# Kernel tuning notes

Hardware: AMD Instinct MI355X
Metric: run time of the kernel (lower is better)

## Reference

```python
import jax, jax.numpy as jnp
import numpy as np

MASK_GROUP = 8
RATIO = 0.125
K = max(1, min(MASK_GROUP, round(RATIO * MASK_GROUP)))  # = 1


def sparify_mask(outM):
    # top-k over the mask_group axis, scatter 1.0 at top-k positions
    _, idx = jax.lax.top_k(outM, K)              # [..., K]
    oh = jax.nn.one_hot(idx, outM.shape[-1], dtype=outM.dtype)  # [..., K, G]
    return jnp.sum(oh, axis=-2)                   # [..., G] 0/1 mask


def setup_inputs() -> dict:
    key = jax.random.key(0)
    ks = jax.random.split(key, 7)
    B, S, D, F = 4, 2048, 2048, 8192
    stdv = 1.0 / np.sqrt(F)
    u = lambda k, shape: jax.random.uniform(k, shape, jnp.float32, -stdv, stdv)
    return {
        "x": jax.random.normal(ks[0], (B, S, D), jnp.float32),
        "W1": u(ks[1], (F, D)),
        "b1": u(ks[2], (F,)),
        "Wm": u(ks[3], (MASK_GROUP, D)),
        "bm": u(ks[4], (MASK_GROUP,)),
        "W2": u(ks[5], (D, F)),
        "b2": u(ks[6], (D,)),
    }


def reference(x, W1, b1, Wm, bm, W2, b2):
    F_out = W1.shape[0]
    repeat_num = F_out // MASK_GROUP
    outL = jnp.einsum('bsd,fd->bsf', x, W1) + b1          # [B,S,F]
    outM = jax.nn.softmax(jnp.einsum('bsd,gd->bsg', x, Wm) + bm, axis=-1)  # [B,S,G]
    mask = sparify_mask(outM)                              # [B,S,G]
    gate = jnp.repeat(mask, repeat_num, axis=-1)           # [B,S,F]
    out2 = jax.nn.relu(outL * gate)
    out = jnp.einsum('bsf,df->bsd', out2, W2) + b2         # [B,S,D]
    return out
```

## Files before the change

### kernel.cpp

```cpp
#include <hip/hip_runtime.h>
#include <hip/hip_bf16.h>

#define T_TOK 8192
#define D_DIM 2048
#define F_DIM 8192
#define G_NUM 8
#define GF    1024
#define GATE_Q 16
#define GATE_D 128

typedef __attribute__((ext_vector_type(8))) short bf16x8;
typedef __attribute__((ext_vector_type(4))) float f32x4;

__device__ __forceinline__ void async_load16(const void* g, void* l) {
    __builtin_amdgcn_global_load_lds(
        (const __attribute__((address_space(1))) unsigned int*)g,
        (__attribute__((address_space(3))) unsigned int*)l, 16, 0, 0);
}

__device__ __forceinline__ unsigned short f2bf(float f) {
    unsigned int u = __float_as_uint(f);
    unsigned int r = (u + 0x7fffu + ((u >> 16) & 1u)) >> 16;
    return (unsigned short)r;
}

__device__ __forceinline__ uint2 pack4(float4 v) {
    union { __hip_bfloat162 b; unsigned u; } c0, c1;
    c0.b = __float22bfloat162_rn({v.x, v.y});
    c1.b = __float22bfloat162_rn({v.z, v.w});
    uint2 r; r.x = c0.u; r.y = c1.u; return r;
}

__device__ __forceinline__ void stage_f32_64(const float* src, char* rowBase,
                                             int sbase, int rmask) {
#pragma unroll
    for (int i = 0; i < 4; ++i) {
        float4 v0 = *(const float4*)(src + i * 8);
        float4 v1 = *(const float4*)(src + i * 8 + 4);
        uint2 p0 = pack4(v0), p1 = pack4(v1);
        uint4 w; w.x = p0.x; w.y = p0.y; w.z = p1.x; w.w = p1.y;
        *(uint4*)(rowBase + ((sbase + i) ^ rmask) * 16) = w;
    }
}


__global__ void zero_cnt_kernel(int* __restrict__ cnt) {
    if (threadIdx.x < G_NUM) cnt[threadIdx.x] = 0;
}

__global__ __launch_bounds__(256)
void convert_kernel(const float* __restrict__ src, unsigned short* __restrict__ dst, int n) {
    int i = (blockIdx.x * 256 + threadIdx.x) * 8;
    if (i >= n) return;
    float4 a = *(const float4*)(src + i);
    float4 b = *(const float4*)(src + i + 4);
    uint2 p0 = pack4(a), p1 = pack4(b);
    uint4 o; o.x = p0.x; o.y = p0.y; o.z = p1.x; o.w = p1.y;
    *(uint4*)(dst + i) = o;
}

template <bool WRITE_XB>
__global__ __launch_bounds__(64)
void gate_partial_kernel(const float* __restrict__ x, const float* __restrict__ Wm,
                         unsigned short* __restrict__ xb, double* __restrict__ part) {
    const int q     = blockIdx.x;
    const int t     = blockIdx.y;
    const int lane  = threadIdx.x;
    const int tok0  = t * 64;
    const int kbase = q * GATE_D;

    __shared__ float wmS[8][GATE_D];
    __shared__ float xs[64][68];

    for (int i = lane * 4; i < 8 * GATE_D; i += 64 * 4) {
        int g = i >> 7, d = i & (GATE_D - 1);
        *(float4*)&wmS[g][d] = *(const float4*)(Wm + (size_t)g * D_DIM + kbase + d);
    }

    double acc[8] = {0, 0, 0, 0, 0, 0, 0, 0};

    const int srow = lane >> 2;
    const int scol = (lane & 3) * 4;

    float4 v[16];
#define LOAD_CHUNK(dbase_)                                                        \
    _Pragma("unroll") for (int it = 0; it < 4; ++it)                              \
    _Pragma("unroll") for (int ci = 0; ci < 4; ++ci) {                            \
        int row = it * 16 + srow;                                                 \
        int col = ci * 16 + scol;                                                 \
        v[it * 4 + ci] = *(const float4*)(x + (size_t)(tok0 + row) * D_DIM +      \
                                          kbase + (dbase_) + col);                \
    }

    LOAD_CHUNK(0)
    __syncthreads();

    for (int s = 0; s < 2; ++s) {
        const int dbase = s * 64;
#pragma unroll
        for (int it = 0; it < 4; ++it)
#pragma unroll
            for (int ci = 0; ci < 4; ++ci) {
                int row = it * 16 + srow;
                int col = ci * 16 + scol;
                *(float4*)&xs[row][col] = v[it * 4 + ci];
                if (WRITE_XB) {
                    uint2 p = pack4(v[it * 4 + ci]);
                    *(uint2*)(xb + (size_t)(tok0 + row) * D_DIM + kbase + dbase + col) = p;
                }
            }
        __syncthreads();
        if (s < 1) { LOAD_CHUNK(dbase + 64) }
#pragma unroll
        for (int j4 = 0; j4 < 16; ++j4) {
            float4 xv = *(const float4*)&xs[lane][j4 * 4];
#pragma unroll
            for (int g = 0; g < 8; ++g) {
                float4 wv = *(const float4*)&wmS[g][dbase + j4 * 4];
                acc[g] += (double)xv.x * (double)wv.x;
                acc[g] += (double)xv.y * (double)wv.y;
                acc[g] += (double)xv.z * (double)wv.z;
                acc[g] += (double)xv.w * (double)wv.w;
            }
        }
        __syncthreads();
    }
#undef LOAD_CHUNK

    double* dst = part + (((size_t)t * GATE_Q + q) * 64 + lane) * 8;
#pragma unroll
    for (int g = 0; g < 8; ++g) dst[g] = acc[g];
}

__global__ __launch_bounds__(64)
void gate_combine_kernel(const double* __restrict__ part, const float* __restrict__ bm,
                         int* __restrict__ cnt, int* __restrict__ bucket) {
    int tok = blockIdx.x * 64 + threadIdx.x;
    int t = tok >> 6, L = tok & 63;
    double s[8];
#pragma unroll
    for (int g = 0; g < 8; ++g) s[g] = (double)bm[g];
#pragma unroll
    for (int q = 0; q < GATE_Q; ++q) {
        const double* p = part + (((size_t)t * GATE_Q + q) * 64 + L) * 8;
#pragma unroll
        for (int g = 0; g < 8; ++g) s[g] += p[g];
    }
    double best = s[0]; int bg = 0;
#pragma unroll
    for (int g = 1; g < 8; ++g)
        if (s[g] > best) { best = s[g]; bg = g; }
    int pos = atomicAdd(&cnt[bg], 1);
    bucket[bg * T_TOK + pos] = tok;
}

template <int KDIM, bool IS_G1, bool A_BF16, bool B_BF16>
__global__ __launch_bounds__(256)
void mfma_gemm(const void* __restrict__ Aop, const void* __restrict__ Bop,
               const float* __restrict__ bias,
               const int* __restrict__ cnt, const int* __restrict__ bucket,
               unsigned short* __restrict__ outH, float* __restrict__ outF) {
    const int g  = blockIdx.z;
    const int n  = cnt[g];
    constexpr int NX = IS_G1 ? (GF / 128) : (D_DIM / 128);
    const int l = blockIdx.y * NX + blockIdx.x;
    const int t0  = ((l & 7) + 8 * (l / (8 * NX))) * 128;
    const int nx0 = ((l >> 3) % NX) * 128;
    if (t0 >= n) return;
    const int tid  = threadIdx.x;
    const int lane = tid & 63;
    const int wv   = tid >> 6;

    __shared__ int toks[128];
    __shared__ __align__(16) unsigned short As[128 * 64];
    __shared__ __align__(16) unsigned short Bs[128 * 64];

    if (tid < 128) {
        int r = t0 + tid;
        if (r >= n) r = n - 1;
        toks[tid] = bucket[g * T_TOK + r];
    }
    __syncthreads();

    const size_t bstride = IS_G1 ? (size_t)KDIM : (size_t)F_DIM;
    const size_t brow0   = IS_G1 ? (size_t)(g * GF + nx0) : (size_t)nx0;
    const size_t bcol    = IS_G1 ? 0 : (size_t)(g * GF);

    const int arow = tid >> 3;
    const int segg = (tid & 7) ^ (arow & 7);
    const unsigned short* aP[4]; const unsigned short* bP[4];
    char* ldsA = (char*)As + tid * 16;
    char* ldsB = (char*)Bs + tid * 16;
    if (A_BF16) {
        const unsigned short* Ab = (const unsigned short*)Aop;
#pragma unroll
        for (int j = 0; j < 4; ++j)
            aP[j] = Ab + (size_t)toks[arow + 32 * j] * KDIM + segg * 8;
    }
    if (B_BF16) {
        const unsigned short* Bb = (const unsigned short*)Bop;
#pragma unroll
        for (int j = 0; j < 4; ++j)
            bP[j] = Bb + (brow0 + arow + 32 * j) * bstride + bcol + segg * 8;
    }

    const int frw = tid >> 1;
    const int fs  = tid & 1;
    const float* aF = nullptr; const float* bF = nullptr;
    char* ldsAf = (char*)As + frw * 128;
    char* ldsBf = (char*)Bs + frw * 128;
    if (!A_BF16) aF = (const float*)Aop + (size_t)toks[frw] * KDIM + fs * 32;
    if (!B_BF16) bF = (const float*)Bop + (brow0 + frw) * bstride + bcol + fs * 32;

    f32x4 acc[4][4];
#pragma unroll
    for (int mi = 0; mi < 4; ++mi)
#pragma unroll
        for (int ni = 0; ni < 4; ++ni)
            acc[mi][ni] = (f32x4){0.f, 0.f, 0.f, 0.f};

    const int wr   = (wv >> 1) * 64;
    const int wc   = (wv & 1) * 64;
    const int frow = lane & 15;
    const int kh   = lane >> 4;
    const int xm   = frow & 7;
    const char* aBase = (const char*)As + (size_t)(wr + frow) * 128;
    const char* bBase = (const char*)Bs + (size_t)(wc + frow) * 128;

    for (int k0 = 0; k0 < KDIM; k0 += 64) {
        __syncthreads();
        if (A_BF16) {
#pragma unroll
            for (int j = 0; j < 4; ++j) async_load16(aP[j] + k0, ldsA + j * 4096);
        }
        if (B_BF16) {
#pragma unroll
            for (int j = 0; j < 4; ++j) async_load16(bP[j] + k0, ldsB + j * 4096);
        }
        if (!A_BF16) stage_f32_64(aF + k0, ldsAf, fs * 4, frw & 7);
        if (!B_BF16) stage_f32_64(bF + k0, ldsBf, fs * 4, frw & 7);
        __syncthreads();
#pragma unroll
        for (int kk = 0; kk < 2; ++kk) {
            const int so = ((kk * 4 + kh) ^ xm) * 16;
            bf16x8 af[4], bfr[4];
#pragma unroll
            for (int mi = 0; mi < 4; ++mi)
                af[mi] = *(const bf16x8*)(aBase + mi * 2048 + so);
#pragma unroll
            for (int ni = 0; ni < 4; ++ni)
                bfr[ni] = *(const bf16x8*)(bBase + ni * 2048 + so);
#pragma unroll
            for (int mi = 0; mi < 4; ++mi)
#pragma unroll
                for (int ni = 0; ni < 4; ++ni)
                    acc[mi][ni] = __builtin_amdgcn_mfma_f32_16x16x32_bf16(
                        af[mi], bfr[ni], acc[mi][ni], 0, 0, 0);
        }
    }

    const float* bptr = bias + (IS_G1 ? (g * GF + nx0) : nx0);
    float bv[4];
#pragma unroll
    for (int ni = 0; ni < 4; ++ni) bv[ni] = bptr[wc + ni * 16 + frow];

#pragma unroll
    for (int mi = 0; mi < 4; ++mi) {
#pragma unroll
        for (int v = 0; v < 4; ++v) {
            int r = wr + mi * 16 + kh * 4 + v;
            if (t0 + r < n) {
                int tok = toks[r];
                if (IS_G1) {
                    unsigned short* dst = outH + (size_t)tok * GF + nx0 + wc + frow;
#pragma unroll
                    for (int ni = 0; ni < 4; ++ni) {
                        float o = fmaxf(acc[mi][ni][v] + bv[ni], 0.f);
                        dst[ni * 16] = f2bf(o);
                    }
                } else {
                    float* dst = outF + (size_t)tok * D_DIM + nx0 + wc + frow;
#pragma unroll
                    for (int ni = 0; ni < 4; ++ni)
                        dst[ni * 16] = acc[mi][ni][v] + bv[ni];
                }
            }
        }
    }
}

extern "C" void kernel_launch(void* const* d_in, const int* in_sizes, int n_in,
                              void* d_out, int out_size, void* d_ws, size_t ws_size,
                              hipStream_t stream) {
    const float* x  = (const float*)d_in[0];
    const float* W1 = (const float*)d_in[1];
    const float* b1 = (const float*)d_in[2];
    const float* Wm = (const float*)d_in[3];
    const float* bm = (const float*)d_in[4];
    const float* W2 = (const float*)d_in[5];
    const float* b2 = (const float*)d_in[6];
    float* out = (float*)d_out;

    int* cnt    = (int*)d_ws;
    int* bucket = (int*)((char*)d_ws + 1024);
    double* part = (double*)((char*)d_ws + (1 << 19));
    unsigned short* Hb  = (unsigned short*)((char*)d_ws + (1 << 19));
    unsigned short* xb  = Hb  + (size_t)T_TOK * GF;
    unsigned short* W1b = xb  + (size_t)T_TOK * D_DIM;
    unsigned short* W2b = W1b + (size_t)F_DIM * D_DIM;

    const bool fast = ws_size >= 117964800ull;
    const bool mid  = ws_size >= 50855936ull;
    const int NCVT = T_TOK * D_DIM;

    zero_cnt_kernel<<<1, 64, 0, stream>>>(cnt);
    if (fast || mid)
        gate_partial_kernel<true><<<dim3(GATE_Q, 128), 64, 0, stream>>>(x, Wm, xb, part);
    else
        gate_partial_kernel<false><<<dim3(GATE_Q, 128), 64, 0, stream>>>(x, Wm, nullptr, part);
    gate_combine_kernel<<<T_TOK / 64, 64, 0, stream>>>(part, bm, cnt, bucket);

    if (fast) {
        convert_kernel<<<NCVT / (256 * 8), 256, 0, stream>>>(W1, W1b, NCVT);
        convert_kernel<<<NCVT / (256 * 8), 256, 0, stream>>>(W2, W2b, NCVT);
        mfma_gemm<D_DIM, true, true, true><<<dim3(GF / 128, T_TOK / 128, G_NUM), 256, 0, stream>>>(
            xb, W1b, b1, cnt, bucket, Hb, nullptr);
        mfma_gemm<GF, false, true, true><<<dim3(D_DIM / 128, T_TOK / 128, G_NUM), 256, 0, stream>>>(
            Hb, W2b, b2, cnt, bucket, nullptr, out);
    } else if (mid) {
        mfma_gemm<D_DIM, true, true, false><<<dim3(GF / 128, T_TOK / 128, G_NUM), 256, 0, stream>>>(
            xb, W1, b1, cnt, bucket, Hb, nullptr);
        mfma_gemm<GF, false, true, false><<<dim3(D_DIM / 128, T_TOK / 128, G_NUM), 256, 0, stream>>>(
            Hb, W2, b2, cnt, bucket, nullptr, out);
    } else {
        mfma_gemm<D_DIM, true, false, false><<<dim3(GF / 128, T_TOK / 128, G_NUM), 256, 0, stream>>>(
            x, W1, b1, cnt, bucket, Hb, nullptr);
        mfma_gemm<GF, false, true, false><<<dim3(D_DIM / 128, T_TOK / 128, G_NUM), 256, 0, stream>>>(
            Hb, W2, b2, cnt, bucket, nullptr, out);
    }
}
```

Measured before the change: 420.1 us.

## Double-buffer LDS tiles with async prefetch in bf16 grouped GEMM

Adds a two-stage LDS ring for the all-bf16 GEMM path. The next K tile's async global-to-LDS loads are issued before computing the current tile, and there is one barrier per iteration instead of two. MFMA sections are wrapped in s_setprio, and the grouped tile-index swizzle is replaced with plain blockIdx mapping. LDS use doubles, which may lower occupancy, and dropping the swizzle may reduce L2 reuse.

Measured after the change: 419.3 us. Within noise of the previous version (-0.2%).

```diff
diff --git a/kernel.cpp b/kernel.cpp
--- a/kernel.cpp
+++ b/kernel.cpp
@@ -162,18 +162,16 @@
                unsigned short* __restrict__ outH, float* __restrict__ outF) {
     const int g  = blockIdx.z;
     const int n  = cnt[g];
-    constexpr int NX = IS_G1 ? (GF / 128) : (D_DIM / 128);
-    const int l = blockIdx.y * NX + blockIdx.x;
-    const int t0  = ((l & 7) + 8 * (l / (8 * NX))) * 128;
-    const int nx0 = ((l >> 3) % NX) * 128;
+    const int t0 = blockIdx.y * 128;
     if (t0 >= n) return;
+    const int nx0 = blockIdx.x * 128;
     const int tid  = threadIdx.x;
     const int lane = tid & 63;
     const int wv   = tid >> 6;
 
     __shared__ int toks[128];
-    __shared__ __align__(16) unsigned short As[128 * 64];
-    __shared__ __align__(16) unsigned short Bs[128 * 64];
+    __shared__ __align__(16) unsigned short As[2][128 * 64];
+    __shared__ __align__(16) unsigned short Bs[2][128 * 64];
 
     if (tid < 128) {
         int r = t0 + tid;
@@ -224,38 +222,66 @@
     const int frow = lane & 15;
     const int kh   = lane >> 4;
     const int xm   = frow & 7;
-    const char* aBase = (const char*)As + (size_t)(wr + frow) * 128;
-    const char* bBase = (const char*)Bs + (size_t)(wc + frow) * 128;
-
-    for (int k0 = 0; k0 < KDIM; k0 += 64) {
-        __syncthreads();
-        if (A_BF16) {
-#pragma unroll
-            for (int j = 0; j < 4; ++j) async_load16(aP[j] + k0, ldsA + j * 4096);
-        }
-        if (B_BF16) {
-#pragma unroll
-            for (int j = 0; j < 4; ++j) async_load16(bP[j] + k0, ldsB + j * 4096);
-        }
-        if (!A_BF16) stage_f32_64(aF + k0, ldsAf, fs * 4, frw & 7);
-        if (!B_BF16) stage_f32_64(bF + k0, ldsBf, fs * 4, frw & 7);
-        __syncthreads();
+
+    auto compute_tile = [&](int buf) {
+        const char* aB = (const char*)As + buf * 16384 + (size_t)(wr + frow) * 128;
+        const char* bB = (const char*)Bs + buf * 16384 + (size_t)(wc + frow) * 128;
+        __builtin_amdgcn_s_setprio(1);
 #pragma unroll
         for (int kk = 0; kk < 2; ++kk) {
             const int so = ((kk * 4 + kh) ^ xm) * 16;
             bf16x8 af[4], bfr[4];
 #pragma unroll
             for (int mi = 0; mi < 4; ++mi)
-                af[mi] = *(const bf16x8*)(aBase + mi * 2048 + so);
+                af[mi] = *(const bf16x8*)(aB + mi * 2048 + so);
 #pragma unroll
             for (int ni = 0; ni < 4; ++ni)
-                bfr[ni] = *(const bf16x8*)(bBase + ni * 2048 + so);
+                bfr[ni] = *(const bf16x8*)(bB + ni * 2048 + so);
 #pragma unroll
             for (int mi = 0; mi < 4; ++mi)
 #pragma unroll
                 for (int ni = 0; ni < 4; ++ni)
                     acc[mi][ni] = __builtin_amdgcn_mfma_f32_16x16x32_bf16(
                         af[mi], bfr[ni], acc[mi][ni], 0, 0, 0);
+        }
+        __builtin_amdgcn_s_setprio(0);
+    };
+
+    if constexpr (A_BF16 && B_BF16) {
+#pragma unroll
+        for (int j = 0; j < 4; ++j) {
+            async_load16(aP[j], ldsA + j * 4096);
+            async_load16(bP[j], ldsB + j * 4096);
+        }
+        __syncthreads();
+        int cur = 0;
+        for (int k0 = 0; k0 < KDIM - 64; k0 += 64) {
+            const int nb = cur ^ 1;
+#pragma unroll
+            for (int j = 0; j < 4; ++j) {
+                async_load16(aP[j] + k0 + 64, ldsA + nb * 16384 + j * 4096);
+                async_load16(bP[j] + k0 + 64, ldsB + nb * 16384 + j * 4096);
+            }
+            compute_tile(cur);
+            __syncthreads();
+            cur = nb;
+        }
+        compute_tile(cur);
+    } else {
+        for (int k0 = 0; k0 < KDIM; k0 += 64) {
+            __syncthreads();
+            if (A_BF16) {
+#pragma unroll
+                for (int j = 0; j < 4; ++j) async_load16(aP[j] + k0, ldsA + j * 4096);
+            }
+            if (B_BF16) {
+#pragma unroll
+                for (int j = 0; j < 4; ++j) async_load16(bP[j] + k0, ldsB + j * 4096);
+            }
+            if (!A_BF16) stage_f32_64(aF + k0, ldsAf, fs * 4, frw & 7);
+            if (!B_BF16) stage_f32_64(bF + k0, ldsBf, fs * 4, frw & 7);
+            __syncthreads();
+            compute_tile(0);
         }
     }
 
```
